# Kernel optimization log

Hardware: AMD Instinct MI355X
Metric: run time of the kernel (lower is better)

The kernel has to match this reference:

```python
import jax, jax.numpy as jnp
import numpy as np

LORA_SCALE = 0.5
LAYER_IDX = 0
NUM_ADAPTERS = 8

def setup_inputs() -> dict:
    key = jax.random.key(0)
    ks = jax.random.split(key, 11)
    T, H, I, A, L, R = 2048, 4096, 11008, NUM_ADAPTERS, 1, 16
    s_base = 1.0 / np.sqrt(H)
    s_down = 1.0 / np.sqrt(I)
    return {
        "x": jax.random.normal(ks[0], (T, H), jnp.float32),
        "gate_w": jax.random.normal(ks[1], (I, H), jnp.float32) * s_base,
        "up_w": jax.random.normal(ks[2], (I, H), jnp.float32) * s_base,
        "down_w": jax.random.normal(ks[3], (H, I), jnp.float32) * s_down,
        "gate_wa": jax.random.normal(ks[4], (A, L, R, H), jnp.float32) * s_base,
        "gate_wb": jax.random.normal(ks[5], (A, L, I, R), jnp.float32) * 0.01,
        "up_wa": jax.random.normal(ks[6], (A, L, R, H), jnp.float32) * s_base,
        "up_wb": jax.random.normal(ks[7], (A, L, I, R), jnp.float32) * 0.01,
        "down_wa": jax.random.normal(ks[8], (A, L, R, I), jnp.float32) * s_down,
        "down_wb": jax.random.normal(ks[9], (A, L, H, R), jnp.float32) * 0.01,
        "indices": jax.random.randint(ks[10], (T,), 0, A, jnp.int64),
    }

def _add_lora(y, x_in, wa, wb, idx, scale):
    # wa: [A, L, r, in], wb: [A, L, out, r]; per-token adapter gather (BGMV)
    wa_t = wa[idx, LAYER_IDX]          # [T, r, in]
    wb_t = wb[idx, LAYER_IDX]          # [T, out, r]
    v = jnp.einsum('ti,tri->tr', x_in, wa_t)     # [T, r]
    return y + scale * jnp.einsum('tr,tor->to', v, wb_t)

def reference(x, gate_w, up_w, down_w, gate_wa, gate_wb, up_wa, up_wb, down_wa, down_wb, indices):
    gate = x @ gate_w.T                                   # [T, I]
    gate = _add_lora(gate, x, gate_wa, gate_wb, indices, LORA_SCALE)
    gate = jax.nn.silu(gate)
    up = x @ up_w.T                                       # [T, I]
    up = _add_lora(up, x, up_wa, up_wb, indices, LORA_SCALE)
    t = gate * up                                         # [T, I]
    down = t @ down_w.T                                   # [T, H]
    down = _add_lora(down, t, down_wa, down_wb, indices, LORA_SCALE)
    return down
```

## Files before the change

kernel.cpp:

```cpp
#include <hip/hip_runtime.h>
#include <hip/hip_bf16.h>
#include <cstdint>


#define T_TOK 2048
#define H_DIM 4096
#define I_DIM 11008
#define R_LORA 16
#define KA1 4352
#define KA2 11136

typedef __bf16 bf16x8 __attribute__((ext_vector_type(8)));
typedef float f32x4 __attribute__((ext_vector_type(4)));

__device__ __forceinline__ float bf2f(unsigned short u) {
    union { unsigned int i; float f; } v;
    v.i = ((unsigned int)u) << 16;
    return v.f;
}
__device__ __forceinline__ unsigned short f2bf(float f) {
    __bf16 b = (__bf16)f;
    unsigned short u;
    __builtin_memcpy(&u, &b, 2);
    return u;
}
__device__ __forceinline__ void cvt8(const float* s, unsigned short* d) {
    float4 a = reinterpret_cast<const float4*>(s)[0];
    float4 b = reinterpret_cast<const float4*>(s)[1];
    uint4 o;
    o.x = (unsigned)f2bf(a.x) | ((unsigned)f2bf(a.y) << 16);
    o.y = (unsigned)f2bf(a.z) | ((unsigned)f2bf(a.w) << 16);
    o.z = (unsigned)f2bf(b.x) | ((unsigned)f2bf(b.y) << 16);
    o.w = (unsigned)f2bf(b.z) | ((unsigned)f2bf(b.w) << 16);
    *reinterpret_cast<uint4*>(d) = o;
}
__device__ __forceinline__ void gload_lds16(const void* g, void* l) {
    __builtin_amdgcn_global_load_lds(
        (const __attribute__((address_space(1))) void*)g,
        (__attribute__((address_space(3))) void*)l,
        16, 0, 0);
}

__global__ __launch_bounds__(256) void cvt_rows(
    const float* __restrict__ src, unsigned short* __restrict__ dst, int K)
{
    const int row = blockIdx.x;
    const int tid = threadIdx.x;
    const float* s = src + (size_t)row * K;
    unsigned short* d = dst + (size_t)row * K;
    for (int k = tid * 8; k < K; k += 256 * 8) cvt8(s + k, d + k);
}

__global__ __launch_bounds__(256) void build_xa_x(
    const float* __restrict__ x, unsigned short* __restrict__ xa)
{
    const int t = blockIdx.x;
    const int tid = threadIdx.x;
    const float* s = x + (size_t)t * H_DIM;
    unsigned short* d = xa + (size_t)t * KA1;
    for (int k = tid * 8; k < H_DIM; k += 2048) cvt8(s + k, d + k);
}

__global__ __launch_bounds__(256) void fill_xa_aug(
    const float* __restrict__ V, const int* __restrict__ idx,
    unsigned short* __restrict__ xa)
{
    const int t = blockIdx.x;
    const int tid = threadIdx.x;
    const int a = (tid & 127) >> 4;
    const float val = (a == idx[t]) ? 0.5f * V[(size_t)t * 256 + tid] : 0.f;
    xa[(size_t)t * KA1 + H_DIM + tid] = f2bf(val);
}

__global__ __launch_bounds__(128) void fill_ta(
    const float* __restrict__ V, const int* __restrict__ idx,
    unsigned short* __restrict__ t_aug)
{
    const int t = blockIdx.x;
    const int tid = threadIdx.x;
    const int a = tid >> 4;
    const float val = (a == idx[t]) ? 0.5f * V[(size_t)t * 128 + tid] : 0.f;
    t_aug[(size_t)t * KA2 + I_DIM + tid] = f2bf(val);
}

__global__ __launch_bounds__(256) void build_w_aug(
    const float* __restrict__ w, const float* __restrict__ wb,
    unsigned short* __restrict__ dst,
    int Nrows, int Ksrc, int Kdst, int self_off, int zero_off)
{
    const int c = blockIdx.x;
    const int tid = threadIdx.x;
    const float* src = w + (size_t)c * Ksrc;
    unsigned short* d = dst + (size_t)c * Kdst;
    for (int k = tid * 8; k < Ksrc; k += 256 * 8) cvt8(src + k, d + k);
    if (tid < 128) {
        const int a = tid >> 4, r = tid & 15;
        const float v = wb[(((size_t)a * Nrows) + c) * R_LORA + r];
        d[self_off + tid] = f2bf(v);
        if (zero_off >= 0) d[zero_off + tid] = 0;
    }
}

__global__ __launch_bounds__(512) void gemm_thin(
    const unsigned short* __restrict__ A, int lda,
    const unsigned short* __restrict__ B, int ldb,
    float* __restrict__ out, int N, int K)
{
    __shared__ __align__(16) unsigned short As[128][64];
    __shared__ __align__(16) unsigned short Bs[128][64];

    const int tid = threadIdx.x;
    const int lane = tid & 63;
    const int wid = tid >> 6;
    const int wr = wid >> 2;
    const int wc = wid & 3;
    const int fr = lane & 15;
    const int hi = lane >> 4;
    const int fsw = fr & 7;

    const int bm0 = blockIdx.y * 128;
    const int bn0 = blockIdx.x * 128;

    const int srow = tid >> 3;
    const int sslot = tid & 7;
    const int gcol = (sslot ^ (srow & 7)) * 8;
    const unsigned short* Ag = A + (size_t)(bm0 + srow) * lda + gcol;
    const unsigned short* Bg = B + (size_t)(bn0 + srow) * ldb + gcol;
    const size_t halfA = (size_t)64 * lda;
    const size_t halfB = (size_t)64 * ldb;

    f32x4 acc[4][2] = {};

    for (int kt = 0; kt < K; kt += 64) {
        gload_lds16(Ag + kt,         &As[srow][sslot * 8]);
        gload_lds16(Ag + halfA + kt, &As[64 + srow][sslot * 8]);
        gload_lds16(Bg + kt,         &Bs[srow][sslot * 8]);
        gload_lds16(Bg + halfB + kt, &Bs[64 + srow][sslot * 8]);
        __syncthreads();
        #pragma unroll
        for (int kk = 0; kk < 2; ++kk) {
            bf16x8 a_[4], b_[2];
            #pragma unroll
            for (int m = 0; m < 4; ++m)
                a_[m] = *reinterpret_cast<const bf16x8*>(
                    &As[wr * 64 + m * 16 + fr][((kk * 4 + hi) ^ fsw) * 8]);
            #pragma unroll
            for (int n = 0; n < 2; ++n)
                b_[n] = *reinterpret_cast<const bf16x8*>(
                    &Bs[wc * 32 + n * 16 + fr][((kk * 4 + hi) ^ fsw) * 8]);
            #pragma unroll
            for (int m = 0; m < 4; ++m)
                #pragma unroll
                for (int n = 0; n < 2; ++n)
                    acc[m][n] = __builtin_amdgcn_mfma_f32_16x16x32_bf16(
                        a_[m], b_[n], acc[m][n], 0, 0, 0);
        }
        __syncthreads();
    }

    const int orow0 = bm0 + wr * 64 + hi * 4;
    const int ocol0 = bn0 + wc * 32 + fr;
    #pragma unroll
    for (int m = 0; m < 4; ++m)
        #pragma unroll
        for (int j = 0; j < 4; ++j) {
            const int row = orow0 + m * 16 + j;
            #pragma unroll
            for (int n = 0; n < 2; ++n)
                out[(size_t)row * N + ocol0 + n * 16] = acc[m][n][j];
        }
}

__global__ __launch_bounds__(512, 2) void gemm_fused_gu(
    const unsigned short* __restrict__ A,
    const unsigned short* __restrict__ Bg,
    const unsigned short* __restrict__ Bu,
    unsigned short* __restrict__ Tout)
{
    __shared__ __align__(16) unsigned short lds[2][512][64];

    const int tid = threadIdx.x;
    const int lane = tid & 63;
    const int wid = tid >> 6;
    const int wr = wid >> 1;
    const int wc = wid & 1;
    const int fr = lane & 15;
    const int hi = lane >> 4;
    const int fsw = fr & 7;

    const int bm0 = (blockIdx.x & 7) * 256;
    const int bn0 = (blockIdx.x >> 3) * 128;

    const int srow = tid >> 3;
    const int sslot = tid & 7;
    const int gcol = (sslot ^ (srow & 7)) * 8;
    const unsigned short* Ap  = A  + (size_t)(bm0 + srow) * KA1 + gcol;
    const unsigned short* Bgp = Bg + (size_t)(bn0 + srow) * KA1 + gcol;
    const unsigned short* Bup = Bu + (size_t)(bn0 + srow) * KA1 + gcol;

    f32x4 accg[4][4] = {};
    f32x4 accu[4][4] = {};

    const int nt = KA1 / 64;
    int cur = 0;

    auto stage_AB = [&](int buf, int kt) {
        #pragma unroll
        for (int q = 0; q < 4; ++q)
            gload_lds16(Ap + (size_t)(q * 64) * KA1 + kt, &lds[buf][q * 64 + srow][sslot * 8]);
        gload_lds16(Bgp + kt,                      &lds[buf][256 + srow][sslot * 8]);
        gload_lds16(Bgp + (size_t)64 * KA1 + kt,   &lds[buf][320 + srow][sslot * 8]);
    };
    auto stage_U = [&](int buf, int kt) {
        gload_lds16(Bup + kt,                      &lds[buf][384 + srow][sslot * 8]);
        gload_lds16(Bup + (size_t)64 * KA1 + kt,   &lds[buf][448 + srow][sslot * 8]);
    };

    stage_AB(0, 0);
    stage_U(0, 0);
    asm volatile("s_waitcnt vmcnt(2)" ::: "memory");
    __builtin_amdgcn_s_barrier();

    for (int t = 0; t < nt; ++t) {
        const int nxt = cur ^ 1;
        const bool last = (t == nt - 1);
        const int ktn = (t + 1) * 64;

        bf16x8 a_[4][2], b_[4][2];
        #pragma unroll
        for (int m = 0; m < 4; ++m)
            #pragma unroll
            for (int k = 0; k < 2; ++k)
                a_[m][k] = *reinterpret_cast<const bf16x8*>(
                    &lds[cur][wr * 64 + m * 16 + fr][((k * 4 + hi) ^ fsw) * 8]);
        #pragma unroll
        for (int n = 0; n < 4; ++n)
            #pragma unroll
            for (int k = 0; k < 2; ++k)
                b_[n][k] = *reinterpret_cast<const bf16x8*>(
                    &lds[cur][256 + wc * 64 + n * 16 + fr][((k * 4 + hi) ^ fsw) * 8]);
        if (!last) stage_AB(nxt, ktn);
        if (last) asm volatile("s_waitcnt vmcnt(0)" ::: "memory");
        else      asm volatile("s_waitcnt vmcnt(6)" ::: "memory");
        __builtin_amdgcn_s_barrier();
        asm volatile("s_waitcnt lgkmcnt(0)" ::: "memory");
        __builtin_amdgcn_sched_barrier(0);
        __builtin_amdgcn_s_setprio(1);
        #pragma unroll
        for (int m = 0; m < 4; ++m)
            #pragma unroll
            for (int n = 0; n < 4; ++n)
                #pragma unroll
                for (int k = 0; k < 2; ++k)
                    accg[m][n] = __builtin_amdgcn_mfma_f32_16x16x32_bf16(
                        a_[m][k], b_[n][k], accg[m][n], 0, 0, 0);
        __builtin_amdgcn_s_setprio(0);
        __builtin_amdgcn_s_barrier();

        #pragma unroll
        for (int n = 0; n < 4; ++n)
            #pragma unroll
            for (int k = 0; k < 2; ++k)
                b_[n][k] = *reinterpret_cast<const bf16x8*>(
                    &lds[cur][384 + wc * 64 + n * 16 + fr][((k * 4 + hi) ^ fsw) * 8]);
        if (!last) stage_U(nxt, ktn);
        if (!last) asm volatile("s_waitcnt vmcnt(2)" ::: "memory");
        __builtin_amdgcn_s_barrier();
        asm volatile("s_waitcnt lgkmcnt(0)" ::: "memory");
        __builtin_amdgcn_sched_barrier(0);
        __builtin_amdgcn_s_setprio(1);
        #pragma unroll
        for (int m = 0; m < 4; ++m)
            #pragma unroll
            for (int n = 0; n < 4; ++n)
                #pragma unroll
                for (int k = 0; k < 2; ++k)
                    accu[m][n] = __builtin_amdgcn_mfma_f32_16x16x32_bf16(
                        a_[m][k], b_[n][k], accu[m][n], 0, 0, 0);
        __builtin_amdgcn_s_setprio(0);
        __builtin_amdgcn_s_barrier();

        cur = nxt;
    }

    const int orow0 = bm0 + wr * 64 + hi * 4;
    const int ocol0 = bn0 + wc * 64 + fr;
    #pragma unroll
    for (int m = 0; m < 4; ++m)
        #pragma unroll
        for (int j = 0; j < 4; ++j) {
            const int row = orow0 + m * 16 + j;
            #pragma unroll
            for (int n = 0; n < 4; ++n) {
                const float g = accg[m][n][j];
                const float u = accu[m][n][j];
                const float sg = g / (1.f + __expf(-g));
                Tout[(size_t)row * KA2 + ocol0 + n * 16] = f2bf(sg * u);
            }
        }
}

__global__ __launch_bounds__(512, 2) void gemm_down(
    const unsigned short* __restrict__ A,
    const unsigned short* __restrict__ B,
    float* __restrict__ out)
{
    __shared__ __align__(16) unsigned short lds[3][384][64];

    const int tid = threadIdx.x;
    const int lane = tid & 63;
    const int wid = tid >> 6;
    const int wr = wid >> 1;
    const int wc = wid & 1;
    const int fr = lane & 15;
    const int hi = lane >> 4;
    const int fsw = fr & 7;

    const int bm0 = (blockIdx.x & 7) * 256;
    const int bn0 = (blockIdx.x >> 3) * 128;

    const int srow = tid >> 3;
    const int sslot = tid & 7;
    const int gcol = (sslot ^ (srow & 7)) * 8;
    const unsigned short* Ap = A + (size_t)(bm0 + srow) * KA2 + gcol;
    const unsigned short* Bp = B + (size_t)(bn0 + srow) * KA2 + gcol;

    f32x4 acc[4][4] = {};

    const int nt = KA2 / 64;
    int cur = 0, st = 2;

    auto stage_A = [&](int buf, int kt) {
        #pragma unroll
        for (int q = 0; q < 4; ++q)
            gload_lds16(Ap + (size_t)(q * 64) * KA2 + kt, &lds[buf][q * 64 + srow][sslot * 8]);
    };
    auto stage_B = [&](int buf, int kt) {
        gload_lds16(Bp + kt,                     &lds[buf][256 + srow][sslot * 8]);
        gload_lds16(Bp + (size_t)64 * KA2 + kt,  &lds[buf][320 + srow][sslot * 8]);
    };

    stage_A(0, 0);  stage_B(0, 0);
    stage_A(1, 64); stage_B(1, 64);
    asm volatile("s_waitcnt vmcnt(6)" ::: "memory");
    __builtin_amdgcn_s_barrier();

    for (int t = 0; t < nt; ++t) {
        const bool has2 = (t + 2 < nt);
        const int ktn = (t + 2) * 64;

        bf16x8 a_[4][2], b_[4][2];
        #pragma unroll
        for (int m = 0; m < 4; ++m)
            #pragma unroll
            for (int k = 0; k < 2; ++k)
                a_[m][k] = *reinterpret_cast<const bf16x8*>(
                    &lds[cur][wr * 64 + m * 16 + fr][((k * 4 + hi) ^ fsw) * 8]);
        #pragma unroll
        for (int n = 0; n < 2; ++n)
            #pragma unroll
            for (int k = 0; k < 2; ++k)
                b_[n][k] = *reinterpret_cast<const bf16x8*>(
                    &lds[cur][256 + wc * 64 + n * 16 + fr][((k * 4 + hi) ^ fsw) * 8]);
        if (has2) stage_A(st, ktn);
        __builtin_amdgcn_s_barrier();
        asm volatile("s_waitcnt lgkmcnt(0)" ::: "memory");
        __builtin_amdgcn_sched_barrier(0);
        __builtin_amdgcn_s_setprio(1);
        #pragma unroll
        for (int m = 0; m < 4; ++m)
            #pragma unroll
            for (int n = 0; n < 2; ++n)
                #pragma unroll
                for (int k = 0; k < 2; ++k)
                    acc[m][n] = __builtin_amdgcn_mfma_f32_16x16x32_bf16(
                        a_[m][k], b_[n][k], acc[m][n], 0, 0, 0);
        __builtin_amdgcn_s_setprio(0);
        __builtin_amdgcn_s_barrier();

        #pragma unroll
        for (int n = 0; n < 2; ++n)
            #pragma unroll
            for (int k = 0; k < 2; ++k)
                b_[n][k] = *reinterpret_cast<const bf16x8*>(
                    &lds[cur][256 + wc * 64 + (n + 2) * 16 + fr][((k * 4 + hi) ^ fsw) * 8]);
        if (has2) stage_B(st, ktn);
        if (t == nt - 2) asm volatile("s_waitcnt vmcnt(0)" ::: "memory");
        else if (t < nt - 2) asm volatile("s_waitcnt vmcnt(6)" ::: "memory");
        __builtin_amdgcn_s_barrier();
        asm volatile("s_waitcnt lgkmcnt(0)" ::: "memory");
        __builtin_amdgcn_sched_barrier(0);
        __builtin_amdgcn_s_setprio(1);
        #pragma unroll
        for (int m = 0; m < 4; ++m)
            #pragma unroll
            for (int n = 0; n < 2; ++n)
                #pragma unroll
                for (int k = 0; k < 2; ++k)
                    acc[m][n + 2] = __builtin_amdgcn_mfma_f32_16x16x32_bf16(
                        a_[m][k], b_[n][k], acc[m][n + 2], 0, 0, 0);
        __builtin_amdgcn_s_setprio(0);
        __builtin_amdgcn_s_barrier();

        cur = (cur == 2) ? 0 : cur + 1;
        st  = (st == 2) ? 0 : st + 1;
    }

    const int orow0 = bm0 + wr * 64 + hi * 4;
    const int ocol0 = bn0 + wc * 64 + fr;
    #pragma unroll
    for (int m = 0; m < 4; ++m)
        #pragma unroll
        for (int j = 0; j < 4; ++j) {
            const int row = orow0 + m * 16 + j;
            #pragma unroll
            for (int n = 0; n < 4; ++n)
                out[(size_t)row * H_DIM + ocol0 + n * 16] = acc[m][n][j];
        }
}

extern "C" void kernel_launch(void* const* d_in, const int* in_sizes, int n_in,
                              void* d_out, int out_size, void* d_ws, size_t ws_size,
                              hipStream_t stream)
{
    const float* x       = (const float*)d_in[0];
    const float* gate_w  = (const float*)d_in[1];
    const float* up_w    = (const float*)d_in[2];
    const float* down_w  = (const float*)d_in[3];
    const float* gate_wa = (const float*)d_in[4];
    const float* gate_wb = (const float*)d_in[5];
    const float* up_wa   = (const float*)d_in[6];
    const float* up_wb   = (const float*)d_in[7];
    const float* down_wa = (const float*)d_in[8];
    const float* down_wb = (const float*)d_in[9];
    const int*   indices = (const int*)d_in[10];
    float* out = (float*)d_out;

    char* ws = (char*)d_ws;
    size_t off = 0;
    auto alloc = [&](size_t bytes) {
        char* p = ws + off;
        off += (bytes + 255) & ~(size_t)255;
        return p;
    };
    unsigned short* xa     = (unsigned short*)alloc((size_t)T_TOK * KA1 * 2);
    unsigned short* wg_aug = (unsigned short*)alloc((size_t)I_DIM * KA1 * 2);
    unsigned short* wu_aug = (unsigned short*)alloc((size_t)I_DIM * KA1 * 2);
    unsigned short* t_aug  = (unsigned short*)alloc((size_t)T_TOK * KA2 * 2);
    unsigned short* wab_gu = (unsigned short*)alloc((size_t)256 * H_DIM * 2);
    float* Vgu = (float*)t_aug;
    float* Vd  = (float*)wab_gu;
    unsigned short* wd_aug = wu_aug;
    unsigned short* wab_d  = wu_aug + (size_t)H_DIM * KA2;

    cvt_rows<<<128, 256, 0, stream>>>(gate_wa, wab_gu, H_DIM);
    cvt_rows<<<128, 256, 0, stream>>>(up_wa, wab_gu + (size_t)128 * H_DIM, H_DIM);
    build_xa_x<<<T_TOK, 256, 0, stream>>>(x, xa);
    gemm_thin<<<dim3(2, 16), 512, 0, stream>>>(xa, KA1, wab_gu, H_DIM, Vgu, 256, H_DIM);
    fill_xa_aug<<<T_TOK, 256, 0, stream>>>(Vgu, indices, xa);

    build_w_aug<<<I_DIM, 256, 0, stream>>>(gate_w, gate_wb, wg_aug,
                                           I_DIM, H_DIM, KA1, H_DIM, H_DIM + 128);
    build_w_aug<<<I_DIM, 256, 0, stream>>>(up_w, up_wb, wu_aug,
                                           I_DIM, H_DIM, KA1, H_DIM + 128, H_DIM);

    gemm_fused_gu<<<8 * (I_DIM / 128), 512, 0, stream>>>(xa, wg_aug, wu_aug, t_aug);

    cvt_rows<<<128, 256, 0, stream>>>(down_wa, wab_d, I_DIM);
    gemm_thin<<<dim3(1, 16), 512, 0, stream>>>(t_aug, KA2, wab_d, I_DIM, Vd, 128, I_DIM);
    fill_ta<<<T_TOK, 128, 0, stream>>>(Vd, indices, t_aug);
    build_w_aug<<<H_DIM, 256, 0, stream>>>(down_w, down_wb, wd_aug,
                                           H_DIM, I_DIM, KA2, I_DIM, -1);

    gemm_down<<<8 * (H_DIM / 128), 512, 0, stream>>>(t_aug, wd_aug, out);

    (void)in_sizes; (void)n_in; (void)out_size; (void)ws_size;
}
```

Baseline: 1.004 ms.

## Split MFMA phases along K halves to shrink fragment registers and finer interleave

Both GEMM main loops are restructured so each phase loads only one 32-wide K half of the A and B fragments and runs all 16 MFMAs on it, instead of loading the full K=64 fragments up front and splitting by N. The gate/up kernel now has four phases per tile (gate k0, gate k1, up k0, up k1), and global staging is split so A+gate and up loads issue in different phases. The aim is to cut live fragment registers and interleave LDS reads with MFMA work more finely. The cost is more barriers per iteration and retuned vmcnt waits, which could add synchronisation stalls.

```diff
diff --git a/kernel.cpp b/kernel.cpp
--- a/kernel.cpp
+++ b/kernel.cpp
@@ -41,6 +41,15 @@
         16, 0, 0);
 }
 
+#define PH_PRE()                                              \
+    __builtin_amdgcn_s_barrier();                             \
+    asm volatile("s_waitcnt lgkmcnt(0)" ::: "memory");        \
+    __builtin_amdgcn_sched_barrier(0);                        \
+    __builtin_amdgcn_s_setprio(1)
+#define PH_POST()                                             \
+    __builtin_amdgcn_s_setprio(0);                            \
+    __builtin_amdgcn_s_barrier()
+
 __global__ __launch_bounds__(256) void cvt_rows(
     const float* __restrict__ src, unsigned short* __restrict__ dst, int K)
 {
@@ -204,81 +213,95 @@
     const int nt = KA1 / 64;
     int cur = 0;
 
-    auto stage_AB = [&](int buf, int kt) {
+    auto stage_A = [&](int buf, int kt) {
         #pragma unroll
         for (int q = 0; q < 4; ++q)
             gload_lds16(Ap + (size_t)(q * 64) * KA1 + kt, &lds[buf][q * 64 + srow][sslot * 8]);
-        gload_lds16(Bgp + kt,                      &lds[buf][256 + srow][sslot * 8]);
-        gload_lds16(Bgp + (size_t)64 * KA1 + kt,   &lds[buf][320 + srow][sslot * 8]);
+    };
+    auto stage_G = [&](int buf, int kt) {
+        gload_lds16(Bgp + kt,                    &lds[buf][256 + srow][sslot * 8]);
+        gload_lds16(Bgp + (size_t)64 * KA1 + kt, &lds[buf][320 + srow][sslot * 8]);
     };
     auto stage_U = [&](int buf, int kt) {
-        gload_lds16(Bup + kt,                      &lds[buf][384 + srow][sslot * 8]);
-        gload_lds16(Bup + (size_t)64 * KA1 + kt,   &lds[buf][448 + srow][sslot * 8]);
-    };
-
-    stage_AB(0, 0);
-    stage_U(0, 0);
+        gload_lds16(Bup + kt,                    &lds[buf][384 + srow][sslot * 8]);
+        gload_lds16(Bup + (size_t)64 * KA1 + kt, &lds[buf][448 + srow][sslot * 8]);
+    };
+
+    stage_A(0, 0); stage_G(0, 0); stage_U(0, 0);
     asm volatile("s_waitcnt vmcnt(2)" ::: "memory");
     __builtin_amdgcn_s_barrier();
+
+    bf16x8 a0[4], a1[4], b0[4], b1[4];
 
     for (int t = 0; t < nt; ++t) {
         const int nxt = cur ^ 1;
         const bool last = (t == nt - 1);
         const int ktn = (t + 1) * 64;
 
-        bf16x8 a_[4][2], b_[4][2];
-        #pragma unroll
-        for (int m = 0; m < 4; ++m)
-            #pragma unroll
-            for (int k = 0; k < 2; ++k)
-                a_[m][k] = *reinterpret_cast<const bf16x8*>(
-                    &lds[cur][wr * 64 + m * 16 + fr][((k * 4 + hi) ^ fsw) * 8]);
-        #pragma unroll
-        for (int n = 0; n < 4; ++n)
-            #pragma unroll
-            for (int k = 0; k < 2; ++k)
-                b_[n][k] = *reinterpret_cast<const bf16x8*>(
-                    &lds[cur][256 + wc * 64 + n * 16 + fr][((k * 4 + hi) ^ fsw) * 8]);
-        if (!last) stage_AB(nxt, ktn);
+        #pragma unroll
+        for (int m = 0; m < 4; ++m)
+            a0[m] = *reinterpret_cast<const bf16x8*>(
+                &lds[cur][wr * 64 + m * 16 + fr][(hi ^ fsw) * 8]);
+        #pragma unroll
+        for (int n = 0; n < 4; ++n)
+            b0[n] = *reinterpret_cast<const bf16x8*>(
+                &lds[cur][256 + wc * 64 + n * 16 + fr][(hi ^ fsw) * 8]);
+        if (!last) { stage_A(nxt, ktn); stage_G(nxt, ktn); }
+        PH_PRE();
+        #pragma unroll
+        for (int m = 0; m < 4; ++m)
+            #pragma unroll
+            for (int n = 0; n < 4; ++n)
+                accg[m][n] = __builtin_amdgcn_mfma_f32_16x16x32_bf16(
+                    a0[m], b0[n], accg[m][n], 0, 0, 0);
+        PH_POST();
+
+        #pragma unroll
+        for (int m = 0; m < 4; ++m)
+            a1[m] = *reinterpret_cast<const bf16x8*>(
+                &lds[cur][wr * 64 + m * 16 + fr][(((4 + hi)) ^ fsw) * 8]);
+        #pragma unroll
+        for (int n = 0; n < 4; ++n)
+            b1[n] = *reinterpret_cast<const bf16x8*>(
+                &lds[cur][256 + wc * 64 + n * 16 + fr][(((4 + hi)) ^ fsw) * 8]);
+        if (!last) stage_U(nxt, ktn);
         if (last) asm volatile("s_waitcnt vmcnt(0)" ::: "memory");
-        else      asm volatile("s_waitcnt vmcnt(6)" ::: "memory");
-        __builtin_amdgcn_s_barrier();
-        asm volatile("s_waitcnt lgkmcnt(0)" ::: "memory");
-        __builtin_amdgcn_sched_barrier(0);
-        __builtin_amdgcn_s_setprio(1);
-        #pragma unroll
-        for (int m = 0; m < 4; ++m)
-            #pragma unroll
-            for (int n = 0; n < 4; ++n)
-                #pragma unroll
-                for (int k = 0; k < 2; ++k)
-                    accg[m][n] = __builtin_amdgcn_mfma_f32_16x16x32_bf16(
-                        a_[m][k], b_[n][k], accg[m][n], 0, 0, 0);
-        __builtin_amdgcn_s_setprio(0);
-        __builtin_amdgcn_s_barrier();
-
-        #pragma unroll
-        for (int n = 0; n < 4; ++n)
-            #pragma unroll
-            for (int k = 0; k < 2; ++k)
-                b_[n][k] = *reinterpret_cast<const bf16x8*>(
-                    &lds[cur][384 + wc * 64 + n * 16 + fr][((k * 4 + hi) ^ fsw) * 8]);
-        if (!last) stage_U(nxt, ktn);
+        else      asm volatile("s_waitcnt vmcnt(8)" ::: "memory");
+        PH_PRE();
+        #pragma unroll
+        for (int m = 0; m < 4; ++m)
+            #pragma unroll
+            for (int n = 0; n < 4; ++n)
+                accg[m][n] = __builtin_amdgcn_mfma_f32_16x16x32_bf16(
+                    a1[m], b1[n], accg[m][n], 0, 0, 0);
+        PH_POST();
+
+        #pragma unroll
+        for (int n = 0; n < 4; ++n)
+            b0[n] = *reinterpret_cast<const bf16x8*>(
+                &lds[cur][384 + wc * 64 + n * 16 + fr][(hi ^ fsw) * 8]);
+        PH_PRE();
+        #pragma unroll
+        for (int m = 0; m < 4; ++m)
+            #pragma unroll
+            for (int n = 0; n < 4; ++n)
+                accu[m][n] = __builtin_amdgcn_mfma_f32_16x16x32_bf16(
+                    a0[m], b0[n], accu[m][n], 0, 0, 0);
+        PH_POST();
+
+        #pragma unroll
+        for (int n = 0; n < 4; ++n)
+            b1[n] = *reinterpret_cast<const bf16x8*>(
+                &lds[cur][384 + wc * 64 + n * 16 + fr][(((4 + hi)) ^ fsw) * 8]);
         if (!last) asm volatile("s_waitcnt vmcnt(2)" ::: "memory");
-        __builtin_amdgcn_s_barrier();
-        asm volatile("s_waitcnt lgkmcnt(0)" ::: "memory");
-        __builtin_amdgcn_sched_barrier(0);
-        __builtin_amdgcn_s_setprio(1);
-        #pragma unroll
-        for (int m = 0; m < 4; ++m)
-            #pragma unroll
-            for (int n = 0; n < 4; ++n)
-                #pragma unroll
-                for (int k = 0; k < 2; ++k)
-                    accu[m][n] = __builtin_amdgcn_mfma_f32_16x16x32_bf16(
-                        a_[m][k], b_[n][k], accu[m][n], 0, 0, 0);
-        __builtin_amdgcn_s_setprio(0);
-        __builtin_amdgcn_s_barrier();
+        PH_PRE();
+        #pragma unroll
+        for (int m = 0; m < 4; ++m)
+            #pragma unroll
+            for (int n = 0; n < 4; ++n)
+                accu[m][n] = __builtin_amdgcn_mfma_f32_16x16x32_bf16(
+                    a1[m], b1[n], accu[m][n], 0, 0, 0);
+        PH_POST();
 
         cur = nxt;
     }
@@ -336,8 +359,8 @@
             gload_lds16(Ap + (size_t)(q * 64) * KA2 + kt, &lds[buf][q * 64 + srow][sslot * 8]);
     };
     auto stage_B = [&](int buf, int kt) {
-        gload_lds16(Bp + kt,                     &lds[buf][256 + srow][sslot * 8]);
-        gload_lds16(Bp + (size_t)64 * KA2 + kt,  &lds[buf][320 + srow][sslot * 8]);
+        gload_lds16(Bp + kt,                    &lds[buf][256 + srow][sslot * 8]);
+        gload_lds16(Bp + (size_t)64 * KA2 + kt, &lds[buf][320 + srow][sslot * 8]);
     };
 
     stage_A(0, 0);  stage_B(0, 0);
@@ -345,62 +368,49 @@
     asm volatile("s_waitcnt vmcnt(6)" ::: "memory");
     __builtin_amdgcn_s_barrier();
 
+    bf16x8 a0[4], a1[4], b0[4], b1[4];
+
     for (int t = 0; t < nt; ++t) {
         const bool has2 = (t + 2 < nt);
         const int ktn = (t + 2) * 64;
 
-        bf16x8 a_[4][2], b_[4][2];
-        #pragma unroll
-        for (int m = 0; m < 4; ++m)
-            #pragma unroll
-            for (int k = 0; k < 2; ++k)
-                a_[m][k] = *reinterpret_cast<const bf16x8*>(
-                    &lds[cur][wr * 64 + m * 16 + fr][((k * 4 + hi) ^ fsw) * 8]);
-        #pragma unroll
-        for (int n = 0; n < 2; ++n)
-            #pragma unroll
-            for (int k = 0; k < 2; ++k)
-                b_[n][k] = *reinterpret_cast<const bf16x8*>(
-                    &lds[cur][256 + wc * 64 + n * 16 + fr][((k * 4 + hi) ^ fsw) * 8]);
+        #pragma unroll
+        for (int m = 0; m < 4; ++m)
+            a0[m] = *reinterpret_cast<const bf16x8*>(
+                &lds[cur][wr * 64 + m * 16 + fr][(hi ^ fsw) * 8]);
+        #pragma unroll
+        for (int n = 0; n < 4; ++n)
+            b0[n] = *reinterpret_cast<const bf16x8*>(
+                &lds[cur][256 + wc * 64 + n * 16 + fr][(hi ^ fsw) * 8]);
         if (has2) stage_A(st, ktn);
-        __builtin_amdgcn_s_barrier();
-        asm volatile("s_waitcnt lgkmcnt(0)" ::: "memory");
-        __builtin_amdgcn_sched_barrier(0);
-        __builtin_amdgcn_s_setprio(1);
-        #pragma unroll
-        for (int m = 0; m < 4; ++m)
-            #pragma unroll
-            for (int n = 0; n < 2; ++n)
-                #pragma unroll
-                for (int k = 0; k < 2; ++k)
-                    acc[m][n] = __builtin_amdgcn_mfma_f32_16x16x32_bf16(
-                        a_[m][k], b_[n][k], acc[m][n], 0, 0, 0);
-        __builtin_amdgcn_s_setprio(0);
-        __builtin_amdgcn_s_barrier();
-
-        #pragma unroll
-        for (int n = 0; n < 2; ++n)
-            #pragma unroll
-            for (int k = 0; k < 2; ++k)
-                b_[n][k] = *reinterpret_cast<const bf16x8*>(
-                    &lds[cur][256 + wc * 64 + (n + 2) * 16 + fr][((k * 4 + hi) ^ fsw) * 8]);
+        PH_PRE();
+        #pragma unroll
+        for (int m = 0; m < 4; ++m)
+            #pragma unroll
+            for (int n = 0; n < 4; ++n)
+                acc[m][n] = __builtin_amdgcn_mfma_f32_16x16x32_bf16(
+                    a0[m], b0[n], acc[m][n], 0, 0, 0);
+        PH_POST();
+
+        #pragma unroll
+        for (int m = 0; m < 4; ++m)
+            a1[m] = *reinterpret_cast<const bf16x8*>(
+                &lds[cur][wr * 64 + m * 16 + fr][(((4 + hi)) ^ fsw) * 8]);
+        #pragma unroll
+        for (int n = 0; n < 4; ++n)
+            b1[n] = *reinterpret_cast<const bf16x8*>(
+                &lds[cur][256 + wc * 64 + n * 16 + fr][(((4 + hi)) ^ fsw) * 8]);
         if (has2) stage_B(st, ktn);
-        if (t == nt - 2) asm volatile("s_waitcnt vmcnt(0)" ::: "memory");
+        if (t == nt - 2)     asm volatile("s_waitcnt vmcnt(0)" ::: "memory");
         else if (t < nt - 2) asm volatile("s_waitcnt vmcnt(6)" ::: "memory");
-        __builtin_amdgcn_s_barrier();
-        asm volatile("s_waitcnt lgkmcnt(0)" ::: "memory");
-        __builtin_amdgcn_sched_barrier(0);
-        __builtin_amdgcn_s_setprio(1);
-        #pragma unroll
-        for (int m = 0; m < 4; ++m)
-            #pragma unroll
-            for (int n = 0; n < 2; ++n)
-                #pragma unroll
-                for (int k = 0; k < 2; ++k)
-                    acc[m][n + 2] = __builtin_amdgcn_mfma_f32_16x16x32_bf16(
-                        a_[m][k], b_[n][k], acc[m][n + 2], 0, 0, 0);
-        __builtin_amdgcn_s_setprio(0);
-        __builtin_amdgcn_s_barrier();
+        PH_PRE();
+        #pragma unroll
+        for (int m = 0; m < 4; ++m)
+            #pragma unroll
+            for (int n = 0; n < 4; ++n)
+                acc[m][n] = __builtin_amdgcn_mfma_f32_16x16x32_bf16(
+                    a1[m], b1[n], acc[m][n], 0, 0, 0);
+        PH_POST();
 
         cur = (cur == 2) ? 0 : cur + 1;
         st  = (st == 2) ? 0 : st + 1;
```

Result: faster. 960.1 us (-4.4%).
